# Optimization experiments

Hardware: AMD Instinct MI355X
Metric: run time of the kernel (lower is better)

Reference implementation:

```python
import jax, jax.numpy as jnp
import numpy as np

N_NODES = 100000
N_EDGES = 1600000
IN_FEATS = 64
HIDDEN = 64
NUM_CLASSES = 40


def setup_inputs() -> dict:
    key = jax.random.key(0)
    ks = jax.random.split(key, 8)
    x = jax.random.normal(ks[0], (N_NODES, IN_FEATS), dtype=jnp.float32)
    edge_index = jax.random.randint(ks[1], (2, N_EDGES), 0, N_NODES, dtype=jnp.int64)
    s = 1.0 / np.sqrt(IN_FEATS)
    W1_l = jax.random.uniform(ks[2], (HIDDEN, IN_FEATS), jnp.float32, -s, s)
    b1 = jnp.zeros((HIDDEN,), jnp.float32)
    W1_r = jax.random.uniform(ks[3], (HIDDEN, IN_FEATS), jnp.float32, -s, s)
    s2 = 1.0 / np.sqrt(HIDDEN)
    W2_l = jax.random.uniform(ks[4], (NUM_CLASSES, HIDDEN), jnp.float32, -s2, s2)
    b2 = jnp.zeros((NUM_CLASSES,), jnp.float32)
    W2_r = jax.random.uniform(ks[5], (NUM_CLASSES, HIDDEN), jnp.float32, -s2, s2)
    return {"x": x, "edge_index": edge_index, "W1_l": W1_l, "b1": b1,
            "W1_r": W1_r, "W2_l": W2_l, "b2": b2, "W2_r": W2_r}


def _sage_conv(x, src, dst, Wl, b, Wr, num_nodes):
    # mean aggregation of source-node features onto target nodes
    msg = x[src]                                           # [E, d] gather
    agg = jax.ops.segment_sum(msg, dst, num_segments=num_nodes)   # [N, d]
    deg = jax.ops.segment_sum(jnp.ones((src.shape[0],), x.dtype), dst,
                              num_segments=num_nodes)      # [N]
    agg = agg / jnp.maximum(deg, 1.0)[:, None]
    # out = lin_l(agg) + lin_r(x)  (PyG SAGEConv: root weight, bias on lin_l)
    return agg @ Wl.T + b + x @ Wr.T


def reference(x, edge_index, W1_l, b1, W1_r, W2_l, b2, W2_r):
    n = x.shape[0]
    src, dst = edge_index[0], edge_index[1]
    h = _sage_conv(x, src, dst, W1_l, b1, W1_r, n)
    h = jax.nn.relu(h)
    # dropout p=0.5 only active in training; reference runs eval mode (identity)
    return _sage_conv(h, src, dst, W2_l, b2, W2_r, n)
```

## Files before the change

### kernel.cpp

```cpp
#include <hip/hip_runtime.h>

#define N_NODES 100000
#define N_EDGES 1600000
#define NCLS 40
#define BIN_SH 8
#define BIN_N 256
#define NBIN ((N_NODES + BIN_N - 1) / BIN_N)
#define BINCAP 4800
#define BKBLK 256
#define BKTHR 1024
#define CHUNK (N_EDGES / BKBLK)
#define SENTINEL N_NODES

typedef __attribute__((ext_vector_type(8))) short s8v;
typedef __attribute__((ext_vector_type(4))) float f4v;

__device__ __forceinline__ unsigned short f2bf(float f) {
    union { float f; unsigned int u; } v; v.f = f;
    unsigned int u = v.u + 0x7FFFu + ((v.u >> 16) & 1u);
    return (unsigned short)(u >> 16);
}
__device__ __forceinline__ float blo(unsigned int u) {
    union { unsigned int u; float f; } v; v.u = u << 16; return v.f;
}
__device__ __forceinline__ float bhi(unsigned int u) {
    union { unsigned int u; float f; } v; v.u = u & 0xFFFF0000u; return v.f;
}

#if __has_builtin(__builtin_amdgcn_cvt_pk_fp8_f32) && __has_builtin(__builtin_amdgcn_cvt_f32_fp8)
#define FP8_HW 1
#else
#define FP8_HW 0
#endif

__device__ __forceinline__ unsigned char enc_e4m3_sw(float f) {
    union { float f; unsigned int u; } v; v.f = f;
    unsigned int s = (v.u >> 24) & 0x80u;
    float af = fabsf(f);
    if (af >= 448.0f) return (unsigned char)(s | 0x7E);
    if (af < 0.015625f) {
        int q = (int)rintf(af * 512.0f);
        return (unsigned char)(s | (q & 7));
    }
    unsigned int n = v.u & 0x7FFFFFFFu;
    n = n + 0x7FFFFu + ((n >> 20) & 1u);
    int e = (int)(n >> 23) - 120;
    unsigned int m = (n >> 20) & 7u;
    if (e <= 0) { int q = (int)rintf(af * 512.0f); return (unsigned char)(s | (q & 7)); }
    if (e > 15) return (unsigned char)(s | 0x7E);
    return (unsigned char)(s | (e << 3) | m);
}
__device__ __forceinline__ float dec_e4m3_sw(unsigned int byte) {
    unsigned int sgn = byte >> 7, e = (byte >> 3) & 15u, m = byte & 7u;
    float mag;
    if (e) { union { unsigned int u; float f; } v; v.u = ((e + 120u) << 23) | (m << 20); mag = v.f; }
    else mag = (float)m * 0.001953125f;
    return sgn ? -mag : mag;
}

__device__ __forceinline__ unsigned int pack4_fp8(float a, float b, float c, float d) {
#if FP8_HW
    unsigned int w = __builtin_amdgcn_cvt_pk_fp8_f32(a, b, 0u, false);
    w = __builtin_amdgcn_cvt_pk_fp8_f32(c, d, w, true);
    return w;
#else
    return (unsigned int)enc_e4m3_sw(a) | ((unsigned int)enc_e4m3_sw(b) << 8) |
           ((unsigned int)enc_e4m3_sw(c) << 16) | ((unsigned int)enc_e4m3_sw(d) << 24);
#endif
}
__device__ __forceinline__ void unpack4_fp8(unsigned int w, float& a, float& b, float& c, float& d) {
#if FP8_HW
    a = __builtin_amdgcn_cvt_f32_fp8(w, 0);
    b = __builtin_amdgcn_cvt_f32_fp8(w, 1);
    c = __builtin_amdgcn_cvt_f32_fp8(w, 2);
    d = __builtin_amdgcn_cvt_f32_fp8(w, 3);
#else
    a = dec_e4m3_sw(w & 255u); b = dec_e4m3_sw((w >> 8) & 255u);
    c = dec_e4m3_sw((w >> 16) & 255u); d = dec_e4m3_sw(w >> 24);
#endif
}

__global__ __launch_bounds__(BKTHR) void k_bucket(
        const int* __restrict__ srcv, const int* __restrict__ dstv,
        int* __restrict__ bcur, int* __restrict__ bedges) {
    __shared__ int cnt4[4][NBIN];
    __shared__ int base[NBIN], lcur[NBIN];
    for (int i = threadIdx.x; i < 4 * NBIN; i += BKTHR) cnt4[i / NBIN][i % NBIN] = 0;
    __syncthreads();
    const int grp = threadIdx.x >> 8;
    const int beg = blockIdx.x * CHUNK;
    const int end = beg + CHUNK;
    for (int e = beg + threadIdx.x; e < end; e += BKTHR) {
        int d = dstv[e]; d = min(max(d, 0), N_NODES - 1);
        atomicAdd(&cnt4[grp][d >> BIN_SH], 1);
    }
    __syncthreads();
    for (int i = threadIdx.x; i < NBIN; i += BKTHR) {
        int c = cnt4[0][i] + cnt4[1][i] + cnt4[2][i] + cnt4[3][i];
        base[i] = atomicAdd(&bcur[i], c);
        lcur[i] = 0;
    }
    __syncthreads();
    for (int e = beg + threadIdx.x; e < end; e += BKTHR) {
        int d = dstv[e]; d = min(max(d, 0), N_NODES - 1);
        int s = srcv[e]; s = min(max(s, 0), N_NODES - 1);
        int b = d >> BIN_SH;
        int slot = atomicAdd(&lcur[b], 1) + base[b];
        if (slot < BINCAP) bedges[b * BINCAP + slot] = ((d & (BIN_N - 1)) << 17) | s;
    }
}

__global__ __launch_bounds__(256) void k_csrfill(
        const int* __restrict__ bcur, const int* __restrict__ bedges,
        int* __restrict__ gcnt, uint2* __restrict__ offdeg,
        int* __restrict__ srcs) {
    __shared__ int dcnt[BIN_N];
    __shared__ int s[BIN_N];
    __shared__ int base_s;
    const int b = blockIdx.x;
    dcnt[threadIdx.x] = 0;
    __syncthreads();
    const int cnt = min(bcur[b], BINCAP);
    for (int e = threadIdx.x; e < cnt; e += 256)
        atomicAdd(&dcnt[bedges[b * BINCAP + e] >> 17], 1);
    __syncthreads();
    int v = dcnt[threadIdx.x];
    int pv = (v + 3) & ~3;
    s[threadIdx.x] = pv;
    __syncthreads();
    int acc = pv;
    for (int off = 1; off < 256; off <<= 1) {
        int t = (threadIdx.x >= off) ? s[threadIdx.x - off] : 0;
        __syncthreads();
        acc += t;
        s[threadIdx.x] = acc;
        __syncthreads();
    }
    if (threadIdx.x == 255) base_s = atomicAdd(gcnt, acc);
    __syncthreads();
    const int gbeg = (acc - pv) + base_s;
    const int node = (b << BIN_SH) + threadIdx.x;
    if (node < N_NODES) offdeg[node] = make_uint2((unsigned)gbeg, (unsigned)v);
    s[threadIdx.x] = gbeg;
    dcnt[threadIdx.x] = 0;
    __syncthreads();
    for (int e = threadIdx.x; e < cnt; e += 256) {
        int val = bedges[b * BINCAP + e];
        int dl = val >> 17;
        int sv = val & 0x1FFFF;
        int slot = atomicAdd(&dcnt[dl], 1);
        srcs[s[dl] + slot] = sv;
    }
    for (int p = v; p < pv; ++p) srcs[gbeg + p] = SENTINEL;
}

__global__ void k_xb(const float* __restrict__ x, unsigned int* __restrict__ xb,
                     unsigned int* __restrict__ h2f8) {
    int i = blockIdx.x * blockDim.x + threadIdx.x;
    int stride = gridDim.x * blockDim.x;
    const int total = N_NODES * 64 / 8;
    for (int t = i; t < total; t += stride) {
        float4 v0 = ((const float4*)x)[t * 2];
        float4 v1 = ((const float4*)x)[t * 2 + 1];
        uint4 o;
        o.x = (unsigned)f2bf(v0.x) | ((unsigned)f2bf(v0.y) << 16);
        o.y = (unsigned)f2bf(v0.z) | ((unsigned)f2bf(v0.w) << 16);
        o.z = (unsigned)f2bf(v1.x) | ((unsigned)f2bf(v1.y) << 16);
        o.w = (unsigned)f2bf(v1.z) | ((unsigned)f2bf(v1.w) << 16);
        ((uint4*)xb)[t] = o;
    }
    uint4 z; z.x = 0u; z.y = 0u; z.z = 0u; z.w = 0u;
    if (i < 8)  ((uint4*)xb)[(size_t)N_NODES * 8 + i] = z;
    if (i >= 8 && i < 12) ((uint4*)h2f8)[(size_t)N_NODES * 4 + (i - 8)] = z;
}

__global__ __launch_bounds__(256) void k_agg(
        const uint2* __restrict__ offdeg, const int* __restrict__ srcs,
        const unsigned short* __restrict__ xb, unsigned short* __restrict__ aggb) {
    const int w = threadIdx.x >> 6;
    const int q = (threadIdx.x >> 4) & 3;
    const int t = threadIdx.x & 15;
    for (int node = blockIdx.x * 4 + w; node < N_NODES; node += gridDim.x * 4) {
        uint2 od = offdeg[node];
        const int beg = (int)od.x;
        const int m = ((int)od.y + 3) >> 2;
        float ax = 0.0f, ay = 0.0f, az = 0.0f, aw = 0.0f;
        int j = q;
        if (j < m) {
            int4 sv = *(const int4*)&srcs[beg + 4 * j];
            while (true) {
                const int4 cur = sv;
                const int jn = j + 4;
                if (jn < m) sv = *(const int4*)&srcs[beg + 4 * jn];
                uint2 u0 = *(const uint2*)&xb[(size_t)cur.x * 64 + t * 4];
                uint2 u1 = *(const uint2*)&xb[(size_t)cur.y * 64 + t * 4];
                uint2 u2 = *(const uint2*)&xb[(size_t)cur.z * 64 + t * 4];
                uint2 u3 = *(const uint2*)&xb[(size_t)cur.w * 64 + t * 4];
                ax += (blo(u0.x) + blo(u1.x)) + (blo(u2.x) + blo(u3.x));
                ay += (bhi(u0.x) + bhi(u1.x)) + (bhi(u2.x) + bhi(u3.x));
                az += (blo(u0.y) + blo(u1.y)) + (blo(u2.y) + blo(u3.y));
                aw += (bhi(u0.y) + bhi(u1.y)) + (bhi(u2.y) + bhi(u3.y));
                if (jn >= m) break;
                j = jn;
            }
        }
        ax += __shfl_xor(ax, 16, 64); ay += __shfl_xor(ay, 16, 64);
        az += __shfl_xor(az, 16, 64); aw += __shfl_xor(aw, 16, 64);
        ax += __shfl_xor(ax, 32, 64); ay += __shfl_xor(ay, 32, 64);
        az += __shfl_xor(az, 32, 64); aw += __shfl_xor(aw, 32, 64);
        if (q == 0) {
            float rd = 1.0f / fmaxf((float)od.y, 1.0f);
            uint2 r;
            r.x = (unsigned)f2bf(ax * rd) | ((unsigned)f2bf(ay * rd) << 16);
            r.y = (unsigned)f2bf(az * rd) | ((unsigned)f2bf(aw * rd) << 16);
            *(uint2*)&aggb[(size_t)node * 64 + t * 4] = r;
        }
    }
}

__global__ __launch_bounds__(256) void k_dense(
        const unsigned short* __restrict__ aggb, const unsigned short* __restrict__ xb,
        const float* __restrict__ W1l, const float* __restrict__ b1,
        const float* __restrict__ W1r,
        const float* __restrict__ W2l, const float* __restrict__ b2,
        const float* __restrict__ W2r,
        unsigned int* __restrict__ h2f8, float* __restrict__ op) {
    __shared__ __align__(16) unsigned short wl1[64][72], wr1[64][72];
    __shared__ __align__(16) unsigned short wl2[48][72], wr2[48][72];
    __shared__ __align__(16) unsigned short hsm[4][16][72];
    for (int idx = threadIdx.x; idx < 64 * 64; idx += 256) {
        int f = idx >> 6, k = idx & 63;
        wl1[f][k] = f2bf(W1l[idx]);
        wr1[f][k] = f2bf(W1r[idx]);
    }
    for (int idx = threadIdx.x; idx < 48 * 64; idx += 256) {
        int c = idx >> 6, k = idx & 63;
        wl2[c][k] = (c < NCLS) ? f2bf(W2l[c * 64 + k]) : (unsigned short)0;
        wr2[c][k] = (c < NCLS) ? f2bf(W2r[c * 64 + k]) : (unsigned short)0;
    }
    __syncthreads();
    const int w   = threadIdx.x >> 6;
    const int l15 = threadIdx.x & 15;
    const int g   = (threadIdx.x >> 4) & 3;
    float b1v[4][4], b2v[3][4];
    #pragma unroll
    for (int ft = 0; ft < 4; ++ft)
        #pragma unroll
        for (int r = 0; r < 4; ++r)
            b1v[ft][r] = b1[16 * ft + 4 * g + r];
    #pragma unroll
    for (int ct = 0; ct < 3; ++ct)
        #pragma unroll
        for (int r = 0; r < 4; ++r) {
            int c = 16 * ct + 4 * g + r;
            b2v[ct][r] = (c < NCLS) ? b2[c] : 0.0f;
        }
    unsigned short* hs = &hsm[w][0][0];
    const int gw = blockIdx.x * 4 + w;
    const int nw = gridDim.x * 4;
    for (int tile = gw; tile < N_NODES / 16; tile += nw) {
        const size_t node = (size_t)tile * 16 + l15;
        s8v aB0 = *(const s8v*)&aggb[node * 64 + 8 * g];
        s8v aB1 = *(const s8v*)&aggb[node * 64 + 32 + 8 * g];
        s8v xB0 = *(const s8v*)&xb[node * 64 + 8 * g];
        s8v xB1 = *(const s8v*)&xb[node * 64 + 32 + 8 * g];
        #pragma unroll
        for (int ft = 0; ft < 4; ++ft) {
            f4v c;
            c[0] = b1v[ft][0]; c[1] = b1v[ft][1]; c[2] = b1v[ft][2]; c[3] = b1v[ft][3];
            const size_t rb = (size_t)(16 * ft + l15) * 144 + 16 * g;
            s8v A0 = *(const s8v*)((const char*)wl1 + rb);
            s8v A1 = *(const s8v*)((const char*)wl1 + rb + 64);
            s8v R0 = *(const s8v*)((const char*)wr1 + rb);
            s8v R1 = *(const s8v*)((const char*)wr1 + rb + 64);
            c = __builtin_amdgcn_mfma_f32_16x16x32_bf16(A0, aB0, c, 0, 0, 0);
            c = __builtin_amdgcn_mfma_f32_16x16x32_bf16(A1, aB1, c, 0, 0, 0);
            c = __builtin_amdgcn_mfma_f32_16x16x32_bf16(R0, xB0, c, 0, 0, 0);
            c = __builtin_amdgcn_mfma_f32_16x16x32_bf16(R1, xB1, c, 0, 0, 0);
            uint2 u;
            u.x = (unsigned)f2bf(fmaxf(c[0], 0.0f)) | ((unsigned)f2bf(fmaxf(c[1], 0.0f)) << 16);
            u.y = (unsigned)f2bf(fmaxf(c[2], 0.0f)) | ((unsigned)f2bf(fmaxf(c[3], 0.0f)) << 16);
            *(uint2*)((char*)hs + l15 * 144 + 32 * ft + 8 * g) = u;
        }
        s8v hB0 = *(const s8v*)((const char*)hs + l15 * 144 + 16 * g);
        s8v hB1 = *(const s8v*)((const char*)hs + l15 * 144 + 64 + 16 * g);
        #pragma unroll
        for (int ct = 0; ct < 3; ++ct) {
            f4v p; p[0] = 0.0f; p[1] = 0.0f; p[2] = 0.0f; p[3] = 0.0f;
            f4v qv;
            qv[0] = b2v[ct][0]; qv[1] = b2v[ct][1]; qv[2] = b2v[ct][2]; qv[3] = b2v[ct][3];
            const size_t rb = (size_t)(16 * ct + l15) * 144 + 16 * g;
            s8v L0 = *(const s8v*)((const char*)wl2 + rb);
            s8v L1 = *(const s8v*)((const char*)wl2 + rb + 64);
            s8v Q0 = *(const s8v*)((const char*)wr2 + rb);
            s8v Q1 = *(const s8v*)((const char*)wr2 + rb + 64);
            p  = __builtin_amdgcn_mfma_f32_16x16x32_bf16(L0, hB0, p, 0, 0, 0);
            p  = __builtin_amdgcn_mfma_f32_16x16x32_bf16(L1, hB1, p, 0, 0, 0);
            qv = __builtin_amdgcn_mfma_f32_16x16x32_bf16(Q0, hB0, qv, 0, 0, 0);
            qv = __builtin_amdgcn_mfma_f32_16x16x32_bf16(Q1, hB1, qv, 0, 0, 0);
            int c0 = 16 * ct + 4 * g;
            if (c0 < NCLS) {
                h2f8[node * 16 + (c0 >> 2)] = pack4_fp8(p[0], p[1], p[2], p[3]);
                float4 o; o.x = qv[0]; o.y = qv[1]; o.z = qv[2]; o.w = qv[3];
                *(float4*)&op[node * NCLS + c0] = o;
            }
        }
    }
}

__global__ __launch_bounds__(256) void k_out(
        const uint2* __restrict__ offdeg, const int* __restrict__ srcs,
        const unsigned int* __restrict__ h2f8, float* __restrict__ out) {
    const int w = threadIdx.x >> 6;
    const int q = (threadIdx.x >> 4) & 3;
    const int t = threadIdx.x & 15;
    for (int node = blockIdx.x * 4 + w; node < N_NODES; node += gridDim.x * 4) {
        uint2 od = offdeg[node];
        const int beg = (int)od.x;
        const int m = ((int)od.y + 3) >> 2;
        float ax = 0.0f, ay = 0.0f, az = 0.0f, aw = 0.0f;
        if (t < 10) {
            int j = q;
            if (j < m) {
                int4 sv = *(const int4*)&srcs[beg + 4 * j];
                while (true) {
                    const int4 cur = sv;
                    const int jn = j + 4;
                    if (jn < m) sv = *(const int4*)&srcs[beg + 4 * jn];
                    unsigned u0 = h2f8[(size_t)cur.x * 16 + t];
                    unsigned u1 = h2f8[(size_t)cur.y * 16 + t];
                    unsigned u2 = h2f8[(size_t)cur.z * 16 + t];
                    unsigned u3 = h2f8[(size_t)cur.w * 16 + t];
                    float a0, b0, c0, d0, a1, b1, c1, d1;
                    float a2, b2, c2, d2, a3, b3, c3, d3;
                    unpack4_fp8(u0, a0, b0, c0, d0);
                    unpack4_fp8(u1, a1, b1, c1, d1);
                    unpack4_fp8(u2, a2, b2, c2, d2);
                    unpack4_fp8(u3, a3, b3, c3, d3);
                    ax += (a0 + a1) + (a2 + a3); ay += (b0 + b1) + (b2 + b3);
                    az += (c0 + c1) + (c2 + c3); aw += (d0 + d1) + (d2 + d3);
                    if (jn >= m) break;
                    j = jn;
                }
            }
        }
        ax += __shfl_xor(ax, 16, 64); ay += __shfl_xor(ay, 16, 64);
        az += __shfl_xor(az, 16, 64); aw += __shfl_xor(aw, 16, 64);
        ax += __shfl_xor(ax, 32, 64); ay += __shfl_xor(ay, 32, 64);
        az += __shfl_xor(az, 32, 64); aw += __shfl_xor(aw, 32, 64);
        if (q == 0 && t < 10) {
            float rd = 1.0f / fmaxf((float)od.y, 1.0f);
            float4 o = *(float4*)&out[(size_t)node * NCLS + t * 4];
            o.x = fmaf(ax, rd, o.x); o.y = fmaf(ay, rd, o.y);
            o.z = fmaf(az, rd, o.z); o.w = fmaf(aw, rd, o.w);
            *(float4*)&out[(size_t)node * NCLS + t * 4] = o;
        }
    }
}

extern "C" void kernel_launch(void* const* d_in, const int* in_sizes, int n_in,
                              void* d_out, int out_size, void* d_ws, size_t ws_size,
                              hipStream_t stream) {
    const float* x   = (const float*)d_in[0];
    const int*   ei  = (const int*)d_in[1];
    const float* W1l = (const float*)d_in[2];
    const float* b1  = (const float*)d_in[3];
    const float* W1r = (const float*)d_in[4];
    const float* W2l = (const float*)d_in[5];
    const float* b2  = (const float*)d_in[6];
    const float* W2r = (const float*)d_in[7];
    float* out = (float*)d_out;

    const int* srcv = ei;
    const int* dstv = ei + N_EDGES;

    int* bcur   = (int*)d_ws;
    int* gcnt   = bcur + 508;
    uint2* offdeg = (uint2*)(bcur + 512);
    int* bedges = (int*)(offdeg + N_NODES);
    int* srcs   = bedges + (size_t)NBIN * BINCAP;
    unsigned short* aggb = (unsigned short*)(srcs + (size_t)N_EDGES + 3 * N_NODES + 16);
    unsigned short* xb   = aggb + (size_t)64 * N_NODES;
    unsigned int*   h2f8 = (unsigned int*)(xb + (size_t)64 * (N_NODES + 1));

    hipMemsetAsync(bcur, 0, 512 * sizeof(int), stream);
    k_bucket<<<BKBLK, BKTHR, 0, stream>>>(srcv, dstv, bcur, bedges);
    k_xb<<<2048, 256, 0, stream>>>(x, (unsigned int*)xb, h2f8);
    k_csrfill<<<NBIN, 256, 0, stream>>>(bcur, bedges, gcnt, offdeg, srcs);
    k_agg<<<2048, 256, 0, stream>>>(offdeg, srcs, xb, aggb);
    k_dense<<<768, 256, 0, stream>>>(aggb, xb, W1l, b1, W1r, W2l, b2, W2r, h2f8, out);
    k_out<<<2048, 256, 0, stream>>>(offdeg, srcs, h2f8, out);
}
```

Baseline: 148.8 us.

## Slice bf16 node features into four 16-wide planes for cache-local gathers

Stores the bf16 copies of x and the layer-1 aggregate as four feature slices of 16 columns each, one plane per slice. In k_agg each block handles a single slice, and block ids are interleaved so that concurrently running blocks touch a smaller plane, which is meant to raise L2/MALL hit rates for the random neighbour gathers. Each wave now works on one node with 16 edge-groups of 4 lanes, so it needs extra shuffle reduction steps. The fp8 layer-2 row stride is also shrunk from 16 to 10 words to cut padding traffic. The cost is 4x more passes over the CSR index and offsets per node, and 8-byte-per-lane gathers spread over more rows.

```diff
diff --git a/kernel.cpp b/kernel.cpp
--- a/kernel.cpp
+++ b/kernel.cpp
@@ -11,6 +11,7 @@
 #define BKTHR 1024
 #define CHUNK (N_EDGES / BKBLK)
 #define SENTINEL N_NODES
+#define NN1 (N_NODES + 1)
 
 typedef __attribute__((ext_vector_type(8))) short s8v;
 typedef __attribute__((ext_vector_type(4))) float f4v;
@@ -154,33 +155,42 @@
     for (int p = v; p < pv; ++p) srcs[gbeg + p] = SENTINEL;
 }
 
-__global__ void k_xb(const float* __restrict__ x, unsigned int* __restrict__ xb,
+__global__ void k_xb(const float* __restrict__ x, unsigned int* __restrict__ xbs,
                      unsigned int* __restrict__ h2f8) {
     int i = blockIdx.x * blockDim.x + threadIdx.x;
     int stride = gridDim.x * blockDim.x;
-    const int total = N_NODES * 64 / 8;
-    for (int t = i; t < total; t += stride) {
-        float4 v0 = ((const float4*)x)[t * 2];
-        float4 v1 = ((const float4*)x)[t * 2 + 1];
+    const int total = N_NODES * 8;
+    for (int tt = i; tt < total; tt += stride) {
+        int node = tt >> 3, sub = tt & 7;
+        int slice = sub >> 1, half = sub & 1;
+        float4 v0 = ((const float4*)x)[tt * 2];
+        float4 v1 = ((const float4*)x)[tt * 2 + 1];
         uint4 o;
         o.x = (unsigned)f2bf(v0.x) | ((unsigned)f2bf(v0.y) << 16);
         o.y = (unsigned)f2bf(v0.z) | ((unsigned)f2bf(v0.w) << 16);
         o.z = (unsigned)f2bf(v1.x) | ((unsigned)f2bf(v1.y) << 16);
         o.w = (unsigned)f2bf(v1.z) | ((unsigned)f2bf(v1.w) << 16);
-        ((uint4*)xb)[t] = o;
+        ((uint4*)xbs)[((size_t)slice * NN1 + node) * 2 + half] = o;
     }
     uint4 z; z.x = 0u; z.y = 0u; z.z = 0u; z.w = 0u;
-    if (i < 8)  ((uint4*)xb)[(size_t)N_NODES * 8 + i] = z;
-    if (i >= 8 && i < 12) ((uint4*)h2f8)[(size_t)N_NODES * 4 + (i - 8)] = z;
+    if (i < 8) {
+        int slice = i >> 1, half = i & 1;
+        ((uint4*)xbs)[((size_t)slice * NN1 + N_NODES) * 2 + half] = z;
+    }
+    if (i >= 16 && i < 26) h2f8[(size_t)N_NODES * 10 + (i - 16)] = 0u;
 }
 
 __global__ __launch_bounds__(256) void k_agg(
         const uint2* __restrict__ offdeg, const int* __restrict__ srcs,
-        const unsigned short* __restrict__ xb, unsigned short* __restrict__ aggb) {
+        const unsigned short* __restrict__ xbs, unsigned short* __restrict__ aggs) {
+    const int lane = threadIdx.x & 63;
     const int w = threadIdx.x >> 6;
-    const int q = (threadIdx.x >> 4) & 3;
-    const int t = threadIdx.x & 15;
-    for (int node = blockIdx.x * 4 + w; node < N_NODES; node += gridDim.x * 4) {
+    const int q = lane >> 2;
+    const int t = lane & 3;
+    const int slice = (blockIdx.x & 7) >> 1;
+    const int cid = ((blockIdx.x >> 3) << 1) | (blockIdx.x & 1);
+    const size_t sb = (size_t)slice * NN1;
+    for (int node = cid * 4 + w; node < N_NODES; node += 2048) {
         uint2 od = offdeg[node];
         const int beg = (int)od.x;
         const int m = ((int)od.y + 3) >> 2;
@@ -190,12 +200,12 @@
             int4 sv = *(const int4*)&srcs[beg + 4 * j];
             while (true) {
                 const int4 cur = sv;
-                const int jn = j + 4;
+                const int jn = j + 16;
                 if (jn < m) sv = *(const int4*)&srcs[beg + 4 * jn];
-                uint2 u0 = *(const uint2*)&xb[(size_t)cur.x * 64 + t * 4];
-                uint2 u1 = *(const uint2*)&xb[(size_t)cur.y * 64 + t * 4];
-                uint2 u2 = *(const uint2*)&xb[(size_t)cur.z * 64 + t * 4];
-                uint2 u3 = *(const uint2*)&xb[(size_t)cur.w * 64 + t * 4];
+                uint2 u0 = *(const uint2*)&xbs[(sb + cur.x) * 16 + t * 4];
+                uint2 u1 = *(const uint2*)&xbs[(sb + cur.y) * 16 + t * 4];
+                uint2 u2 = *(const uint2*)&xbs[(sb + cur.z) * 16 + t * 4];
+                uint2 u3 = *(const uint2*)&xbs[(sb + cur.w) * 16 + t * 4];
                 ax += (blo(u0.x) + blo(u1.x)) + (blo(u2.x) + blo(u3.x));
                 ay += (bhi(u0.x) + bhi(u1.x)) + (bhi(u2.x) + bhi(u3.x));
                 az += (blo(u0.y) + blo(u1.y)) + (blo(u2.y) + blo(u3.y));
@@ -204,6 +214,10 @@
                 j = jn;
             }
         }
+        ax += __shfl_xor(ax, 4, 64);  ay += __shfl_xor(ay, 4, 64);
+        az += __shfl_xor(az, 4, 64);  aw += __shfl_xor(aw, 4, 64);
+        ax += __shfl_xor(ax, 8, 64);  ay += __shfl_xor(ay, 8, 64);
+        az += __shfl_xor(az, 8, 64);  aw += __shfl_xor(aw, 8, 64);
         ax += __shfl_xor(ax, 16, 64); ay += __shfl_xor(ay, 16, 64);
         az += __shfl_xor(az, 16, 64); aw += __shfl_xor(aw, 16, 64);
         ax += __shfl_xor(ax, 32, 64); ay += __shfl_xor(ay, 32, 64);
@@ -213,13 +227,13 @@
             uint2 r;
             r.x = (unsigned)f2bf(ax * rd) | ((unsigned)f2bf(ay * rd) << 16);
             r.y = (unsigned)f2bf(az * rd) | ((unsigned)f2bf(aw * rd) << 16);
-            *(uint2*)&aggb[(size_t)node * 64 + t * 4] = r;
+            *(uint2*)&aggs[(sb + node) * 16 + t * 4] = r;
         }
     }
 }
 
 __global__ __launch_bounds__(256) void k_dense(
-        const unsigned short* __restrict__ aggb, const unsigned short* __restrict__ xb,
+        const unsigned short* __restrict__ aggs, const unsigned short* __restrict__ xbs,
         const float* __restrict__ W1l, const float* __restrict__ b1,
         const float* __restrict__ W1r,
         const float* __restrict__ W2l, const float* __restrict__ b2,
@@ -242,6 +256,9 @@
     const int w   = threadIdx.x >> 6;
     const int l15 = threadIdx.x & 15;
     const int g   = (threadIdx.x >> 4) & 3;
+    const size_t sLo = (size_t)(g >> 1) * NN1;
+    const size_t sHi = (size_t)(2 + (g >> 1)) * NN1;
+    const int off = (g & 1) * 8;
     float b1v[4][4], b2v[3][4];
     #pragma unroll
     for (int ft = 0; ft < 4; ++ft)
@@ -260,10 +277,10 @@
     const int nw = gridDim.x * 4;
     for (int tile = gw; tile < N_NODES / 16; tile += nw) {
         const size_t node = (size_t)tile * 16 + l15;
-        s8v aB0 = *(const s8v*)&aggb[node * 64 + 8 * g];
-        s8v aB1 = *(const s8v*)&aggb[node * 64 + 32 + 8 * g];
-        s8v xB0 = *(const s8v*)&xb[node * 64 + 8 * g];
-        s8v xB1 = *(const s8v*)&xb[node * 64 + 32 + 8 * g];
+        s8v aB0 = *(const s8v*)&aggs[(sLo + node) * 16 + off];
+        s8v aB1 = *(const s8v*)&aggs[(sHi + node) * 16 + off];
+        s8v xB0 = *(const s8v*)&xbs[(sLo + node) * 16 + off];
+        s8v xB1 = *(const s8v*)&xbs[(sHi + node) * 16 + off];
         #pragma unroll
         for (int ft = 0; ft < 4; ++ft) {
             f4v c;
@@ -300,7 +317,7 @@
             qv = __builtin_amdgcn_mfma_f32_16x16x32_bf16(Q1, hB1, qv, 0, 0, 0);
             int c0 = 16 * ct + 4 * g;
             if (c0 < NCLS) {
-                h2f8[node * 16 + (c0 >> 2)] = pack4_fp8(p[0], p[1], p[2], p[3]);
+                h2f8[node * 10 + (c0 >> 2)] = pack4_fp8(p[0], p[1], p[2], p[3]);
                 float4 o; o.x = qv[0]; o.y = qv[1]; o.z = qv[2]; o.w = qv[3];
                 *(float4*)&op[node * NCLS + c0] = o;
             }
@@ -327,10 +344,10 @@
                     const int4 cur = sv;
                     const int jn = j + 4;
                     if (jn < m) sv = *(const int4*)&srcs[beg + 4 * jn];
-                    unsigned u0 = h2f8[(size_t)cur.x * 16 + t];
-                    unsigned u1 = h2f8[(size_t)cur.y * 16 + t];
-                    unsigned u2 = h2f8[(size_t)cur.z * 16 + t];
-                    unsigned u3 = h2f8[(size_t)cur.w * 16 + t];
+                    unsigned u0 = h2f8[(size_t)cur.x * 10 + t];
+                    unsigned u1 = h2f8[(size_t)cur.y * 10 + t];
+                    unsigned u2 = h2f8[(size_t)cur.z * 10 + t];
+                    unsigned u3 = h2f8[(size_t)cur.w * 10 + t];
                     float a0, b0, c0, d0, a1, b1, c1, d1;
                     float a2, b2, c2, d2, a3, b3, c3, d3;
                     unpack4_fp8(u0, a0, b0, c0, d0);
@@ -379,15 +396,15 @@
     uint2* offdeg = (uint2*)(bcur + 512);
     int* bedges = (int*)(offdeg + N_NODES);
     int* srcs   = bedges + (size_t)NBIN * BINCAP;
-    unsigned short* aggb = (unsigned short*)(srcs + (size_t)N_EDGES + 3 * N_NODES + 16);
-    unsigned short* xb   = aggb + (size_t)64 * N_NODES;
-    unsigned int*   h2f8 = (unsigned int*)(xb + (size_t)64 * (N_NODES + 1));
+    unsigned short* aggs = (unsigned short*)(srcs + (size_t)N_EDGES + 3 * N_NODES + 16);
+    unsigned short* xbs  = aggs + (size_t)64 * NN1;
+    unsigned int*   h2f8 = (unsigned int*)(xbs + (size_t)64 * NN1);
 
     hipMemsetAsync(bcur, 0, 512 * sizeof(int), stream);
     k_bucket<<<BKBLK, BKTHR, 0, stream>>>(srcv, dstv, bcur, bedges);
-    k_xb<<<2048, 256, 0, stream>>>(x, (unsigned int*)xb, h2f8);
+    k_xb<<<2048, 256, 0, stream>>>(x, (unsigned int*)xbs, h2f8);
     k_csrfill<<<NBIN, 256, 0, stream>>>(bcur, bedges, gcnt, offdeg, srcs);
-    k_agg<<<2048, 256, 0, stream>>>(offdeg, srcs, xb, aggb);
-    k_dense<<<768, 256, 0, stream>>>(aggb, xb, W1l, b1, W1r, W2l, b2, W2r, h2f8, out);
+    k_agg<<<2048, 256, 0, stream>>>(offdeg, srcs, xbs, aggs);
+    k_dense<<<768, 256, 0, stream>>>(aggs, xbs, W1l, b1, W1r, W2l, b2, W2r, h2f8, out);
     k_out<<<2048, 256, 0, stream>>>(offdeg, srcs, h2f8, out);
 }
```

Measured after the change: 194.6 us. 1.31x slower.
